# Kernel tuning notes

Measured on AMD Instinct MI355X. Metric: run time of the kernel, lower is better.

Reference implementation:

```python
import jax, jax.numpy as jnp
import numpy as np

B, N, D = 8, 128, 256
EPS = 1e-5


def _layernorm(x, g, b):
    m = jnp.mean(x, axis=-1, keepdims=True)
    v = jnp.mean(jnp.square(x - m), axis=-1, keepdims=True)
    return (x - m) * jax.lax.rsqrt(v + EPS) * g + b


def setup_inputs() -> dict:
    key = jax.random.key(0)
    ks = jax.random.split(key, 24)
    s = 0.05  # param init scale
    return {
        "text": jax.random.normal(ks[0], (B, N, D), jnp.float32),
        "adj1": jax.random.uniform(ks[1], (B, N, N), jnp.float32),
        "adj2": jax.random.uniform(ks[2], (B, N, N), jnp.float32),
        "edge1": jax.random.normal(ks[3], (B, N, N, D), jnp.float32) * 0.1,
        "edge2": jax.random.normal(ks[4], (B, N, N, D), jnp.float32) * 0.1,
        "textmask": jnp.ones((B, N), jnp.float32),
        "weight": jax.random.normal(ks[5], (D, D), jnp.float32) * s,
        "bias": jax.random.normal(ks[6], (D,), jnp.float32) * s,
        "gamma": jnp.ones((D,), jnp.float32),
        "beta": jnp.zeros((D,), jnp.float32),
        "fuse1_w": jax.random.normal(ks[7], (2 * D, D), jnp.float32) * s,
        "fuse2_w": jax.random.normal(ks[8], (2 * D, D), jnp.float32) * s,
        "fc3_w": jax.random.normal(ks[9], (2 * D, D), jnp.float32) * s,
        "fc1_w0": jax.random.normal(ks[10], (3 * D, D), jnp.float32) * s,
        "fc1_w1": jax.random.normal(ks[11], (D, 1), jnp.float32) * s,
        "fc1_b1": jnp.zeros((1,), jnp.float32),
        "fc2_w0": jax.random.normal(ks[12], (3 * D, D), jnp.float32) * s,
        "fc2_w1": jax.random.normal(ks[13], (D, 1), jnp.float32) * s,
        "fc2_b1": jnp.zeros((1,), jnp.float32),
        "align_lin": jax.random.normal(ks[14], (D, D), jnp.float32) * s,
        "align_bias": jax.random.normal(ks[15], (D,), jnp.float32) * s,
    }


def reference(text, adj1, adj2, edge1, edge2, textmask, weight, bias, gamma,
              beta, fuse1_w, fuse2_w, fc3_w, fc1_w0, fc1_w1, fc1_b1,
              fc2_w0, fc2_w1, fc2_b1, align_lin, align_bias):
    d = text.shape[-1]
    # ---- SelfAlignment ----
    logits = jnp.einsum('bid,bjd->bij', text @ align_lin, text)
    mask_add = (1.0 - textmask)[:, None, :] * -1e20
    probs = jax.nn.softmax(logits + mask_add, axis=-1)
    outss = jnp.einsum('bij,bjd->bid', probs, text) * textmask[..., None] + align_bias

    # ---- GCN body ----
    out = jax.nn.relu(text @ weight)  # [B,N,D]

    # edge contributions are loop-invariant: precompute once
    # torch cat([x,e]) @ W  ==  x @ W[:d] + e @ W[d:]
    e1_fuse = jnp.einsum('bijd,de->bije', edge1, fuse1_w[d:])
    e2_fuse = jnp.einsum('bijd,de->bije', edge2, fuse2_w[d:])
    e1_fc = jnp.einsum('bijd,de->bije', edge1, fc1_w0[2 * d:])
    e2_fc = jnp.einsum('bijd,de->bije', edge2, fc2_w0[2 * d:])

    denom1 = jnp.sum(adj1, axis=2, keepdims=True) + 1.0  # [B,N,1]
    denom2 = jnp.sum(adj2, axis=2, keepdims=True) + 1.0

    for _ in range(3):  # K = 3
        # text1[b,i,j] = out[b,i]; text2[b,i,j] = out[b,j]
        t_i1 = (out @ fc1_w0[:d])[:, :, None, :]        # text1 part, fc1
        t_j1 = (out @ fc1_w0[d:2 * d])[:, None, :, :]   # text2 part, fc1
        t_i2 = (out @ fc2_w0[:d])[:, :, None, :]
        t_j2 = (out @ fc2_w0[d:2 * d])[:, None, :, :]

        teout = jax.nn.relu((out @ fuse1_w[:d])[:, None, :, :] + e1_fuse)  # [B,N,N,D]
        tein = jax.nn.relu((out @ fuse2_w[:d])[:, None, :, :] + e2_fuse)

        s1 = jax.nn.sigmoid(jax.nn.relu(t_i1 + t_j1 + e1_fc) @ fc1_w1 + fc1_b1)[..., 0]  # [B,N,N]
        s2 = jax.nn.sigmoid(jax.nn.relu(t_i2 + t_j2 + e2_fc) @ fc2_w1 + fc2_b1)[..., 0]

        out1 = jnp.einsum('bij,bijd->bid', adj1 * s1, teout) / denom1
        out2 = jnp.einsum('bij,bijd->bid', adj2 * s2, tein) / denom2

        out = jax.nn.relu(out1 @ fc3_w[:d] + out2 @ fc3_w[d:]) + out + bias
        out = _layernorm(out, gamma, beta)  # dropout = identity (eval)
    return out, outss
```

## Files before the change

### kernel.cpp

```cpp
#include <hip/hip_runtime.h>

typedef unsigned short u16;
typedef unsigned int u32;
typedef __attribute__((ext_vector_type(8))) short bf16x8;
typedef __attribute__((ext_vector_type(4))) float f32x4;

__device__ __forceinline__ u16 f2bf(float f) {
  u32 u = __float_as_uint(f);
  return (u16)((u + 0x7fffu + ((u >> 16) & 1u)) >> 16);
}
__device__ __forceinline__ float bf2f(u16 h) {
  return __uint_as_float(((u32)h) << 16);
}

template<int K, bool OUT_BF16>
__global__ __launch_bounds__(256) void gemm_mfma(
    const float* __restrict__ A, const u16* __restrict__ Bt,
    void* __restrict__ Cv, int Ntot) {
  constexpr int LD = 72;
  __shared__ __align__(16) u16 Asm[128 * LD];
  __shared__ __align__(16) u16 Bsm[256 * LD];
  const int tid = threadIdx.x;
  const int lane = tid & 63;
  const int w = tid >> 6;
  const int m = lane & 15;
  const int q = lane >> 4;
  const int wrow = (w & 1) * 64;
  const int wcol = (w >> 1) * 128;
  const long rowbase = (long)blockIdx.x * 128;
  const long colbase = (long)blockIdx.y * 256;
  f32x4 acc[4][8];
#pragma unroll
  for (int r = 0; r < 4; ++r)
#pragma unroll
    for (int c = 0; c < 8; ++c) acc[r][c] = (f32x4){0.f, 0.f, 0.f, 0.f};

  for (int kc = 0; kc < K / 64; ++kc) {
    const int kb = kc * 64;
#pragma unroll
    for (int it = 0; it < 8; ++it) {
      int f = it * 256 + tid;
      int r = f >> 4, c4 = (f & 15) * 4;
      float4 v = *(const float4*)(A + (rowbase + r) * K + kb + c4);
      ushort4 h;
      h.x = f2bf(v.x); h.y = f2bf(v.y); h.z = f2bf(v.z); h.w = f2bf(v.w);
      *(ushort4*)&Asm[r * LD + c4] = h;
    }
#pragma unroll
    for (int it = 0; it < 8; ++it) {
      int f = it * 256 + tid;
      int c = f >> 3, k8 = (f & 7) * 8;
      *(uint4*)&Bsm[c * LD + k8] =
          *(const uint4*)(Bt + (colbase + c) * K + kb + k8);
    }
    __syncthreads();
#pragma unroll
    for (int s = 0; s < 2; ++s) {
      const int ko = s * 32 + q * 8;
      bf16x8 av[4], bv[8];
#pragma unroll
      for (int r = 0; r < 4; ++r)
        av[r] = *(const bf16x8*)&Asm[(wrow + r * 16 + m) * LD + ko];
#pragma unroll
      for (int c = 0; c < 8; ++c)
        bv[c] = *(const bf16x8*)&Bsm[(wcol + c * 16 + m) * LD + ko];
#pragma unroll
      for (int r = 0; r < 4; ++r)
#pragma unroll
        for (int c = 0; c < 8; ++c)
          acc[r][c] = __builtin_amdgcn_mfma_f32_16x16x32_bf16(
              av[r], bv[c], acc[r][c], 0, 0, 0);
    }
    __syncthreads();
  }
#pragma unroll
  for (int r = 0; r < 4; ++r)
#pragma unroll
    for (int c = 0; c < 8; ++c)
#pragma unroll
      for (int g = 0; g < 4; ++g) {
        long gr = rowbase + wrow + r * 16 + q * 4 + g;
        long gc = colbase + wcol + c * 16 + m;
        float v = acc[r][c][g];
        if (OUT_BF16) ((u16*)Cv)[gr * Ntot + gc] = f2bf(v);
        else          ((float*)Cv)[gr * Ntot + gc] = v;
      }
}

__global__ __launch_bounds__(256) void prep_bt(
    const float* __restrict__ weight, const float* __restrict__ align_lin,
    const float* __restrict__ fuse1_w, const float* __restrict__ fuse2_w,
    const float* __restrict__ fc1_w0, const float* __restrict__ fc2_w0,
    const float* __restrict__ fc3_w,
    u16* BtE1, u16* BtE2, u16* BtW0, u16* BtLoop, u16* BtFc3) {
  int g = blockIdx.x * 256 + threadIdx.x;
  float v;
  u16* dst;
  if (g < 131072) {
    int c = g >> 8, k = g & 255;
    v = (c < 256) ? fuse1_w[(256 + k) * 256 + c]
                  : fc1_w0[(512 + k) * 256 + (c - 256)];
    dst = BtE1 + g;
  } else if (g < 262144) {
    int t = g - 131072;
    int c = t >> 8, k = t & 255;
    v = (c < 256) ? fuse2_w[(256 + k) * 256 + c]
                  : fc2_w0[(512 + k) * 256 + (c - 256)];
    dst = BtE2 + t;
  } else if (g < 393216) {
    int t = g - 262144;
    int c = t >> 8, k = t & 255;
    v = (c < 256) ? weight[k * 256 + c] : align_lin[k * 256 + (c - 256)];
    dst = BtW0 + t;
  } else if (g < 786432) {
    int t = g - 393216;
    int c = t >> 8, k = t & 255;
    int seg = c >> 8, cc = c & 255;
    if      (seg == 0) v = fuse1_w[k * 256 + cc];
    else if (seg == 1) v = fuse2_w[k * 256 + cc];
    else if (seg == 2) v = fc1_w0[k * 256 + cc];
    else if (seg == 3) v = fc1_w0[(256 + k) * 256 + cc];
    else if (seg == 4) v = fc2_w0[k * 256 + cc];
    else               v = fc2_w0[(256 + k) * 256 + cc];
    dst = BtLoop + t;
  } else {
    int t = g - 786432;
    int c = t >> 9, k = t & 511;
    v = fc3_w[k * 256 + c];
    dst = BtFc3 + t;
  }
  *dst = f2bf(v);
}

__global__ __launch_bounds__(256) void relu0_kernel(const float* __restrict__ T0,
                                                    float* __restrict__ outb) {
  long r = blockIdx.x;
  int d = threadIdx.x;
  outb[r * 256 + d] = fmaxf(T0[r * 512 + d], 0.f);
}

__global__ __launch_bounds__(128) void align_kernel(
    const float* __restrict__ text, const float* __restrict__ T0,
    const float* __restrict__ textmask, const float* __restrict__ align_bias,
    float* __restrict__ outss) {
  const int bi = blockIdx.x;
  const int b = bi >> 7;
  const int tid = threadIdx.x;
  __shared__ float ta[256];
  __shared__ float pr[128];
  __shared__ float red[128];
  ta[tid]       = T0[(long)bi * 512 + 256 + tid];
  ta[tid + 128] = T0[(long)bi * 512 + 384 + tid];
  __syncthreads();
  const float* trow = text + (long)(b * 128 + tid) * 256;
  float dot = 0.f;
  for (int d = 0; d < 256; d += 4) {
    float4 t4 = *(const float4*)(trow + d);
    dot += t4.x * ta[d] + t4.y * ta[d + 1] + t4.z * ta[d + 2] + t4.w * ta[d + 3];
  }
  float logit = dot + (1.0f - textmask[b * 128 + tid]) * -1e20f;
  pr[tid] = logit;
  red[tid] = logit;
  __syncthreads();
  for (int off = 64; off; off >>= 1) {
    if (tid < off) red[tid] = fmaxf(red[tid], red[tid + off]);
    __syncthreads();
  }
  float mx = red[0];
  __syncthreads();
  float e = __expf(pr[tid] - mx);
  red[tid] = e;
  __syncthreads();
  for (int off = 64; off; off >>= 1) {
    if (tid < off) red[tid] += red[tid + off];
    __syncthreads();
  }
  float inv = 1.0f / red[0];
  __syncthreads();
  pr[tid] = e * inv;
  __syncthreads();
  const float mi = textmask[bi];
  for (int h = 0; h < 2; ++h) {
    int d = tid + h * 128;
    float s = 0.f;
    for (int j = 0; j < 128; ++j)
      s += pr[j] * text[(long)(b * 128 + j) * 256 + d];
    outss[(long)bi * 256 + d] = s * mi + align_bias[d];
  }
}

__global__ __launch_bounds__(256) void fused_gate(
    const u16* __restrict__ E1, const u16* __restrict__ E2,
    const float* __restrict__ P, const float* __restrict__ adj1,
    const float* __restrict__ adj2, const float* __restrict__ fc1w1,
    const float* __restrict__ fc1b1, const float* __restrict__ fc2w1,
    const float* __restrict__ fc2b1, float* __restrict__ OU12) {
  const int tid = threadIdx.x, lane = tid & 63, w = tid >> 6;
  const int bi = blockIdx.x;
  const int b = bi >> 7, i = bi & 127;
  const int l4 = lane * 4;
  const float4 w1v = *(const float4*)(fc1w1 + l4);
  const float4 w2v = *(const float4*)(fc2w1 + l4);
  const float b1 = fc1b1[0], b2 = fc2b1[0];
  const long rowi = (long)bi * 1536;
  const float4 ti1 = *(const float4*)(P + rowi + 512 + l4);
  const float4 ti2 = *(const float4*)(P + rowi + 1024 + l4);
  float4 acc1 = {0.f, 0.f, 0.f, 0.f}, acc2 = {0.f, 0.f, 0.f, 0.f};
  float da1 = 0.f, da2 = 0.f;
  const long ebase = ((long)b * 16384 + (long)i * 128) * 512;
  const int abase = b * 16384 + i * 128;
  for (int j = w; j < 128; j += 4) {
    const long er = ebase + (long)j * 512;
    ushort4 e1f = *(const ushort4*)(E1 + er + l4);
    ushort4 e1c = *(const ushort4*)(E1 + er + 256 + l4);
    ushort4 e2f = *(const ushort4*)(E2 + er + l4);
    ushort4 e2c = *(const ushort4*)(E2 + er + 256 + l4);
    const long rowj = (long)(b * 128 + j) * 1536;
    float4 of1 = *(const float4*)(P + rowj + l4);
    float4 of2 = *(const float4*)(P + rowj + 256 + l4);
    float4 tj1 = *(const float4*)(P + rowj + 768 + l4);
    float4 tj2 = *(const float4*)(P + rowj + 1280 + l4);
    float a1 = adj1[abase + j], a2 = adj2[abase + j];
    float z1, z2;
    {
      float r0 = fmaxf(ti1.x + tj1.x + bf2f(e1c.x), 0.f);
      float r1 = fmaxf(ti1.y + tj1.y + bf2f(e1c.y), 0.f);
      float r2 = fmaxf(ti1.z + tj1.z + bf2f(e1c.z), 0.f);
      float r3 = fmaxf(ti1.w + tj1.w + bf2f(e1c.w), 0.f);
      z1 = r0 * w1v.x + r1 * w1v.y + r2 * w1v.z + r3 * w1v.w;
      float s0 = fmaxf(ti2.x + tj2.x + bf2f(e2c.x), 0.f);
      float s1_ = fmaxf(ti2.y + tj2.y + bf2f(e2c.y), 0.f);
      float s2_ = fmaxf(ti2.z + tj2.z + bf2f(e2c.z), 0.f);
      float s3_ = fmaxf(ti2.w + tj2.w + bf2f(e2c.w), 0.f);
      z2 = s0 * w2v.x + s1_ * w2v.y + s2_ * w2v.z + s3_ * w2v.w;
    }
#pragma unroll
    for (int off = 32; off; off >>= 1) {
      z1 += __shfl_xor(z1, off);
      z2 += __shfl_xor(z2, off);
    }
    float s1 = a1 / (1.f + __expf(-(z1 + b1)));
    float s2 = a2 / (1.f + __expf(-(z2 + b2)));
    acc1.x += s1 * fmaxf(of1.x + bf2f(e1f.x), 0.f);
    acc1.y += s1 * fmaxf(of1.y + bf2f(e1f.y), 0.f);
    acc1.z += s1 * fmaxf(of1.z + bf2f(e1f.z), 0.f);
    acc1.w += s1 * fmaxf(of1.w + bf2f(e1f.w), 0.f);
    acc2.x += s2 * fmaxf(of2.x + bf2f(e2f.x), 0.f);
    acc2.y += s2 * fmaxf(of2.y + bf2f(e2f.y), 0.f);
    acc2.z += s2 * fmaxf(of2.z + bf2f(e2f.z), 0.f);
    acc2.w += s2 * fmaxf(of2.w + bf2f(e2f.w), 0.f);
    da1 += a1;
    da2 += a2;
  }
  __shared__ float red[4][512];
  __shared__ float dred[4][2];
  *(float4*)&red[w][l4] = acc1;
  *(float4*)&red[w][256 + l4] = acc2;
  if (lane == 0) { dred[w][0] = da1; dred[w][1] = da2; }
  __syncthreads();
  float o1 = red[0][tid] + red[1][tid] + red[2][tid] + red[3][tid];
  float o2 = red[0][256 + tid] + red[1][256 + tid] + red[2][256 + tid] + red[3][256 + tid];
  float d1 = dred[0][0] + dred[1][0] + dred[2][0] + dred[3][0] + 1.f;
  float d2 = dred[0][1] + dred[1][1] + dred[2][1] + dred[3][1] + 1.f;
  OU12[(long)bi * 512 + tid] = o1 / d1;
  OU12[(long)bi * 512 + 256 + tid] = o2 / d2;
}

__global__ __launch_bounds__(256) void ln_kernel(
    const float* __restrict__ Y, const float* __restrict__ prev,
    const float* __restrict__ bias, const float* __restrict__ gamma,
    const float* __restrict__ beta, float* __restrict__ dst) {
  const int row = blockIdx.x, tid = threadIdx.x, lane = tid & 63, w = tid >> 6;
  const long idx = (long)row * 256 + tid;
  float v = fmaxf(Y[idx], 0.f) + prev[idx] + bias[tid];
  float s = v;
#pragma unroll
  for (int off = 32; off; off >>= 1) s += __shfl_xor(s, off);
  __shared__ float wsA[4], wsB[4];
  if (lane == 0) wsA[w] = s;
  __syncthreads();
  float mean = (wsA[0] + wsA[1] + wsA[2] + wsA[3]) * (1.0f / 256.0f);
  float c = v - mean;
  float s2 = c * c;
#pragma unroll
  for (int off = 32; off; off >>= 1) s2 += __shfl_xor(s2, off);
  if (lane == 0) wsB[w] = s2;
  __syncthreads();
  float var = (wsB[0] + wsB[1] + wsB[2] + wsB[3]) * (1.0f / 256.0f);
  dst[idx] = c * rsqrtf(var + 1e-5f) * gamma[tid] + beta[tid];
}

extern "C" void kernel_launch(void* const* d_in, const int* in_sizes, int n_in,
                              void* d_out, int out_size, void* d_ws, size_t ws_size,
                              hipStream_t stream) {
  const float* text      = (const float*)d_in[0];
  const float* adj1      = (const float*)d_in[1];
  const float* adj2      = (const float*)d_in[2];
  const float* edge1     = (const float*)d_in[3];
  const float* edge2     = (const float*)d_in[4];
  const float* textmask  = (const float*)d_in[5];
  const float* weight    = (const float*)d_in[6];
  const float* bias      = (const float*)d_in[7];
  const float* gamma     = (const float*)d_in[8];
  const float* beta      = (const float*)d_in[9];
  const float* fuse1_w   = (const float*)d_in[10];
  const float* fuse2_w   = (const float*)d_in[11];
  const float* fc3_w     = (const float*)d_in[12];
  const float* fc1_w0    = (const float*)d_in[13];
  const float* fc1_w1    = (const float*)d_in[14];
  const float* fc1_b1    = (const float*)d_in[15];
  const float* fc2_w0    = (const float*)d_in[16];
  const float* fc2_w1    = (const float*)d_in[17];
  const float* fc2_b1    = (const float*)d_in[18];
  const float* align_lin = (const float*)d_in[19];
  const float* align_bias= (const float*)d_in[20];
  float* outF = (float*)d_out;

  char* w8 = (char*)d_ws;
  u16*  E1    = (u16*)w8;
  u16*  E2    = E1 + (long)67108864;
  float* P    = (float*)(w8 + 268435456);
  float* T0   = P + 1572864;
  float* OU12 = T0 + 524288;
  float* outb = OU12 + 524288;
  float* Yb   = outb + 262144;
  u16* BtE1   = (u16*)(Yb + 262144);
  u16* BtE2   = BtE1 + 131072;
  u16* BtW0   = BtE2 + 131072;
  u16* BtLoop = BtW0 + 131072;
  u16* BtFc3  = BtLoop + 393216;

  prep_bt<<<3584, 256, 0, stream>>>(weight, align_lin, fuse1_w, fuse2_w,
                                    fc1_w0, fc2_w0, fc3_w,
                                    BtE1, BtE2, BtW0, BtLoop, BtFc3);
  gemm_mfma<256, true><<<dim3(1024, 2), 256, 0, stream>>>(edge1, BtE1, E1, 512);
  gemm_mfma<256, true><<<dim3(1024, 2), 256, 0, stream>>>(edge2, BtE2, E2, 512);
  gemm_mfma<256, false><<<dim3(8, 2), 256, 0, stream>>>(text, BtW0, T0, 512);
  relu0_kernel<<<1024, 256, 0, stream>>>(T0, outb);
  align_kernel<<<1024, 128, 0, stream>>>(text, T0, textmask, align_bias,
                                         outF + 262144);
  for (int it = 0; it < 3; ++it) {
    gemm_mfma<256, false><<<dim3(8, 6), 256, 0, stream>>>(outb, BtLoop, P, 1536);
    fused_gate<<<1024, 256, 0, stream>>>(E1, E2, P, adj1, adj2, fc1_w1, fc1_b1,
                                         fc2_w1, fc2_b1, OU12);
    gemm_mfma<512, false><<<dim3(8, 1), 256, 0, stream>>>(OU12, BtFc3, Yb, 256);
    ln_kernel<<<1024, 256, 0, stream>>>(Yb, outb, bias, gamma, beta,
                                        (it == 2) ? outF : outb);
  }
}
```

Baseline: 835.8 us.

## Pre-convert edges to swizzled bf16 and use LDS-direct loads in edge GEMM

Edge tensors are first converted to bf16 in a swizzled tiled layout, then a new edge GEMM loads tiles straight into LDS with global_load_lds and XOR-swizzled reads. The fused gate kernel is restructured so each 16-lane group handles one j row with 16 channels per lane and a shorter shuffle reduction. The small GEMMs switch to 64-row tiles to launch more blocks. The separate conversion pass adds a full extra read and write of each edge tensor, and the workspace now aliases P with the conversion buffer.

```diff
diff --git a/kernel.cpp b/kernel.cpp
--- a/kernel.cpp
+++ b/kernel.cpp
@@ -4,6 +4,7 @@
 typedef unsigned int u32;
 typedef __attribute__((ext_vector_type(8))) short bf16x8;
 typedef __attribute__((ext_vector_type(4))) float f32x4;
+typedef __attribute__((ext_vector_type(16))) float f32x16;
 
 __device__ __forceinline__ u16 f2bf(float f) {
   u32 u = __float_as_uint(f);
@@ -13,32 +14,130 @@
   return __uint_as_float(((u32)h) << 16);
 }
 
-template<int K, bool OUT_BF16>
+__device__ __forceinline__ void glds16(const void* g, void* l) {
+  __builtin_amdgcn_global_load_lds(
+      (const __attribute__((address_space(1))) unsigned int*)g,
+      (__attribute__((address_space(3))) unsigned int*)l, 16, 0, 0);
+}
+
+__device__ __forceinline__ f32x16 unpack16(const u16* p) {
+  uint4 a = *(const uint4*)p, b = *(const uint4*)(p + 8);
+  f32x16 r;
+  r[0]  = __uint_as_float(a.x << 16); r[1]  = __uint_as_float(a.x & 0xffff0000u);
+  r[2]  = __uint_as_float(a.y << 16); r[3]  = __uint_as_float(a.y & 0xffff0000u);
+  r[4]  = __uint_as_float(a.z << 16); r[5]  = __uint_as_float(a.z & 0xffff0000u);
+  r[6]  = __uint_as_float(a.w << 16); r[7]  = __uint_as_float(a.w & 0xffff0000u);
+  r[8]  = __uint_as_float(b.x << 16); r[9]  = __uint_as_float(b.x & 0xffff0000u);
+  r[10] = __uint_as_float(b.y << 16); r[11] = __uint_as_float(b.y & 0xffff0000u);
+  r[12] = __uint_as_float(b.z << 16); r[13] = __uint_as_float(b.z & 0xffff0000u);
+  r[14] = __uint_as_float(b.w << 16); r[15] = __uint_as_float(b.w & 0xffff0000u);
+  return r;
+}
+
+__global__ __launch_bounds__(256) void convert_edge(
+    const float* __restrict__ src, u16* __restrict__ dst) {
+  int g = blockIdx.x * 256 + threadIdx.x;
+  int kg = g & 7, r = (g >> 3) & 127, kc = (g >> 10) & 3, rt = g >> 12;
+  const float* s = src + ((long)(rt * 128 + r) * 256 + kc * 64 + kg * 8);
+  float4 a = *(const float4*)s, b = *(const float4*)(s + 4);
+  ushort4 lo, hi;
+  lo.x = f2bf(a.x); lo.y = f2bf(a.y); lo.z = f2bf(a.z); lo.w = f2bf(a.w);
+  hi.x = f2bf(b.x); hi.y = f2bf(b.y); hi.z = f2bf(b.z); hi.w = f2bf(b.w);
+  u16* d = dst + (long)rt * 65536 + kc * 16384 + r * 64 + (kg ^ (r & 7)) * 8;
+  *(ushort4*)d = lo;
+  *(ushort4*)(d + 4) = hi;
+}
+
+__global__ __launch_bounds__(256) void gemm_edge(
+    const u16* __restrict__ A, const u16* __restrict__ Bt,
+    u16* __restrict__ E) {
+  __shared__ __align__(16) u16 Asm[8192];
+  __shared__ __align__(16) u16 Bsm[8192];
+  const int tid = threadIdx.x, lane = tid & 63, w = tid >> 6;
+  const int m = lane & 15, q = lane >> 4;
+  const int rt = blockIdx.x >> 2, ct = blockIdx.x & 3;
+  const int wrow = (w & 1) * 64, wcol = (w >> 1) * 64;
+  const char* Ab = (const char*)A + (long)rt * 131072;
+  const char* Bb = (const char*)Bt + (long)ct * 65536;
+  f32x4 acc[4][4];
+#pragma unroll
+  for (int r = 0; r < 4; ++r)
+#pragma unroll
+    for (int c = 0; c < 4; ++c) acc[r][c] = (f32x4){0.f, 0.f, 0.f, 0.f};
+
+  for (int kc = 0; kc < 4; ++kc) {
+#pragma unroll
+    for (int t = 0; t < 4; ++t) {
+      glds16(Ab + kc * 32768 + t * 4096 + tid * 16,
+             (char*)Asm + t * 4096 + tid * 16);
+      glds16(Bb + kc * 16384 + t * 4096 + tid * 16,
+             (char*)Bsm + t * 4096 + tid * 16);
+    }
+    __syncthreads();
+#pragma unroll
+    for (int s = 0; s < 2; ++s) {
+      const int ko2 = (s * 32 + q * 8) * 2;
+      bf16x8 av[4], bv[4];
+#pragma unroll
+      for (int r = 0; r < 4; ++r) {
+        int row = wrow + r * 16 + m;
+        av[r] = *(const bf16x8*)((const char*)Asm + row * 128 +
+                                 (ko2 ^ ((row & 7) * 16)));
+      }
+#pragma unroll
+      for (int c = 0; c < 4; ++c) {
+        int col = wcol + c * 16 + m;
+        bv[c] = *(const bf16x8*)((const char*)Bsm + col * 128 +
+                                 (ko2 ^ ((col & 7) * 16)));
+      }
+#pragma unroll
+      for (int r = 0; r < 4; ++r)
+#pragma unroll
+        for (int c = 0; c < 4; ++c)
+          acc[r][c] = __builtin_amdgcn_mfma_f32_16x16x32_bf16(
+              av[r], bv[c], acc[r][c], 0, 0, 0);
+    }
+    __syncthreads();
+  }
+#pragma unroll
+  for (int r = 0; r < 4; ++r)
+#pragma unroll
+    for (int c = 0; c < 4; ++c)
+#pragma unroll
+      for (int g = 0; g < 4; ++g) {
+        long gr = (long)rt * 128 + wrow + r * 16 + q * 4 + g;
+        int gc = ct * 128 + wcol + c * 16 + m;
+        E[gr * 512 + gc] = f2bf(acc[r][c][g]);
+      }
+}
+
+template<int K, int ROWS, bool OUT_BF16>
 __global__ __launch_bounds__(256) void gemm_mfma(
     const float* __restrict__ A, const u16* __restrict__ Bt,
     void* __restrict__ Cv, int Ntot) {
   constexpr int LD = 72;
-  __shared__ __align__(16) u16 Asm[128 * LD];
+  constexpr int CF = (ROWS == 128) ? 8 : 4;
+  __shared__ __align__(16) u16 Asm[ROWS * LD];
   __shared__ __align__(16) u16 Bsm[256 * LD];
   const int tid = threadIdx.x;
   const int lane = tid & 63;
   const int w = tid >> 6;
   const int m = lane & 15;
   const int q = lane >> 4;
-  const int wrow = (w & 1) * 64;
-  const int wcol = (w >> 1) * 128;
-  const long rowbase = (long)blockIdx.x * 128;
+  const int wrow = (ROWS == 128) ? (w & 1) * 64 : 0;
+  const int wcol = (ROWS == 128) ? (w >> 1) * 128 : w * 64;
+  const long rowbase = (long)blockIdx.x * ROWS;
   const long colbase = (long)blockIdx.y * 256;
-  f32x4 acc[4][8];
+  f32x4 acc[4][CF];
 #pragma unroll
   for (int r = 0; r < 4; ++r)
 #pragma unroll
-    for (int c = 0; c < 8; ++c) acc[r][c] = (f32x4){0.f, 0.f, 0.f, 0.f};
+    for (int c = 0; c < CF; ++c) acc[r][c] = (f32x4){0.f, 0.f, 0.f, 0.f};
 
   for (int kc = 0; kc < K / 64; ++kc) {
     const int kb = kc * 64;
 #pragma unroll
-    for (int it = 0; it < 8; ++it) {
+    for (int it = 0; it < ROWS / 16; ++it) {
       int f = it * 256 + tid;
       int r = f >> 4, c4 = (f & 15) * 4;
       float4 v = *(const float4*)(A + (rowbase + r) * K + kb + c4);
@@ -57,17 +156,17 @@
 #pragma unroll
     for (int s = 0; s < 2; ++s) {
       const int ko = s * 32 + q * 8;
-      bf16x8 av[4], bv[8];
+      bf16x8 av[4], bv[CF];
 #pragma unroll
       for (int r = 0; r < 4; ++r)
         av[r] = *(const bf16x8*)&Asm[(wrow + r * 16 + m) * LD + ko];
 #pragma unroll
-      for (int c = 0; c < 8; ++c)
+      for (int c = 0; c < CF; ++c)
         bv[c] = *(const bf16x8*)&Bsm[(wcol + c * 16 + m) * LD + ko];
 #pragma unroll
       for (int r = 0; r < 4; ++r)
 #pragma unroll
-        for (int c = 0; c < 8; ++c)
+        for (int c = 0; c < CF; ++c)
           acc[r][c] = __builtin_amdgcn_mfma_f32_16x16x32_bf16(
               av[r], bv[c], acc[r][c], 0, 0, 0);
     }
@@ -76,7 +175,7 @@
 #pragma unroll
   for (int r = 0; r < 4; ++r)
 #pragma unroll
-    for (int c = 0; c < 8; ++c)
+    for (int c = 0; c < CF; ++c)
 #pragma unroll
       for (int g = 0; g < 4; ++g) {
         long gr = rowbase + wrow + r * 16 + q * 4 + g;
@@ -94,42 +193,41 @@
     const float* __restrict__ fc3_w,
     u16* BtE1, u16* BtE2, u16* BtW0, u16* BtLoop, u16* BtFc3) {
   int g = blockIdx.x * 256 + threadIdx.x;
-  float v;
-  u16* dst;
-  if (g < 131072) {
-    int c = g >> 8, k = g & 255;
-    v = (c < 256) ? fuse1_w[(256 + k) * 256 + c]
-                  : fc1_w0[(512 + k) * 256 + (c - 256)];
-    dst = BtE1 + g;
-  } else if (g < 262144) {
-    int t = g - 131072;
-    int c = t >> 8, k = t & 255;
-    v = (c < 256) ? fuse2_w[(256 + k) * 256 + c]
-                  : fc2_w0[(512 + k) * 256 + (c - 256)];
-    dst = BtE2 + t;
+  if (g < 262144) {
+    int t = g & 131071;
+    int col = t >> 8, k = t & 255;
+    float v;
+    if (g < 131072)
+      v = (col < 256) ? fuse1_w[(256 + k) * 256 + col]
+                      : fc1_w0[(512 + k) * 256 + (col - 256)];
+    else
+      v = (col < 256) ? fuse2_w[(256 + k) * 256 + col]
+                      : fc2_w0[(512 + k) * 256 + (col - 256)];
+    int ct = col >> 7, cc = col & 127, kc = k >> 6, kk = k & 63;
+    u16* dst = (g < 131072) ? BtE1 : BtE2;
+    dst[ct * 32768 + kc * 8192 + cc * 64 + (kk ^ ((cc & 7) * 8))] = f2bf(v);
   } else if (g < 393216) {
     int t = g - 262144;
     int c = t >> 8, k = t & 255;
-    v = (c < 256) ? weight[k * 256 + c] : align_lin[k * 256 + (c - 256)];
-    dst = BtW0 + t;
+    float v = (c < 256) ? weight[k * 256 + c] : align_lin[k * 256 + (c - 256)];
+    BtW0[t] = f2bf(v);
   } else if (g < 786432) {
     int t = g - 393216;
     int c = t >> 8, k = t & 255;
     int seg = c >> 8, cc = c & 255;
+    float v;
     if      (seg == 0) v = fuse1_w[k * 256 + cc];
     else if (seg == 1) v = fuse2_w[k * 256 + cc];
     else if (seg == 2) v = fc1_w0[k * 256 + cc];
     else if (seg == 3) v = fc1_w0[(256 + k) * 256 + cc];
     else if (seg == 4) v = fc2_w0[k * 256 + cc];
     else               v = fc2_w0[(256 + k) * 256 + cc];
-    dst = BtLoop + t;
+    BtLoop[t] = f2bf(v);
   } else {
     int t = g - 786432;
     int c = t >> 9, k = t & 511;
-    v = fc3_w[k * 256 + c];
-    dst = BtFc3 + t;
-  }
-  *dst = f2bf(v);
+    BtFc3[t] = f2bf(fc3_w[k * 256 + c]);
+  }
 }
 
 __global__ __launch_bounds__(256) void relu0_kernel(const float* __restrict__ T0,
@@ -196,72 +294,78 @@
     const float* __restrict__ fc1b1, const float* __restrict__ fc2w1,
     const float* __restrict__ fc2b1, float* __restrict__ OU12) {
   const int tid = threadIdx.x, lane = tid & 63, w = tid >> 6;
-  const int bi = blockIdx.x;
-  const int b = bi >> 7, i = bi & 127;
-  const int l4 = lane * 4;
-  const float4 w1v = *(const float4*)(fc1w1 + l4);
-  const float4 w2v = *(const float4*)(fc2w1 + l4);
+  const int g16 = lane >> 4, l16 = lane & 15;
+  const int bi = blockIdx.x, b = bi >> 7;
+  const int db = l16 * 16;
+  const long rowi = (long)bi * 1536;
+  const f32x16 w1v = *(const f32x16*)(fc1w1 + db);
+  const f32x16 w2v = *(const f32x16*)(fc2w1 + db);
+  const f32x16 ti1 = *(const f32x16*)(P + rowi + 512 + db);
+  const f32x16 ti2 = *(const f32x16*)(P + rowi + 1024 + db);
   const float b1 = fc1b1[0], b2 = fc2b1[0];
-  const long rowi = (long)bi * 1536;
-  const float4 ti1 = *(const float4*)(P + rowi + 512 + l4);
-  const float4 ti2 = *(const float4*)(P + rowi + 1024 + l4);
-  float4 acc1 = {0.f, 0.f, 0.f, 0.f}, acc2 = {0.f, 0.f, 0.f, 0.f};
+  const long ebase = (long)bi * 65536;
+  const int abase = bi * 128;
+  f32x16 acc1, acc2;
+#pragma unroll
+  for (int dd = 0; dd < 16; ++dd) { acc1[dd] = 0.f; acc2[dd] = 0.f; }
   float da1 = 0.f, da2 = 0.f;
-  const long ebase = ((long)b * 16384 + (long)i * 128) * 512;
-  const int abase = b * 16384 + i * 128;
-  for (int j = w; j < 128; j += 4) {
+
+  for (int t = 0; t < 8; ++t) {
+    const int j = w * 32 + t * 4 + g16;
     const long er = ebase + (long)j * 512;
-    ushort4 e1f = *(const ushort4*)(E1 + er + l4);
-    ushort4 e1c = *(const ushort4*)(E1 + er + 256 + l4);
-    ushort4 e2f = *(const ushort4*)(E2 + er + l4);
-    ushort4 e2c = *(const ushort4*)(E2 + er + 256 + l4);
     const long rowj = (long)(b * 128 + j) * 1536;
-    float4 of1 = *(const float4*)(P + rowj + l4);
-    float4 of2 = *(const float4*)(P + rowj + 256 + l4);
-    float4 tj1 = *(const float4*)(P + rowj + 768 + l4);
-    float4 tj2 = *(const float4*)(P + rowj + 1280 + l4);
+    f32x16 e1cf = unpack16(E1 + er + 256 + db);
+    f32x16 e2cf = unpack16(E2 + er + 256 + db);
+    f32x16 tj1 = *(const f32x16*)(P + rowj + 768 + db);
+    f32x16 tj2 = *(const f32x16*)(P + rowj + 1280 + db);
     float a1 = adj1[abase + j], a2 = adj2[abase + j];
-    float z1, z2;
-    {
-      float r0 = fmaxf(ti1.x + tj1.x + bf2f(e1c.x), 0.f);
-      float r1 = fmaxf(ti1.y + tj1.y + bf2f(e1c.y), 0.f);
-      float r2 = fmaxf(ti1.z + tj1.z + bf2f(e1c.z), 0.f);
-      float r3 = fmaxf(ti1.w + tj1.w + bf2f(e1c.w), 0.f);
-      z1 = r0 * w1v.x + r1 * w1v.y + r2 * w1v.z + r3 * w1v.w;
-      float s0 = fmaxf(ti2.x + tj2.x + bf2f(e2c.x), 0.f);
-      float s1_ = fmaxf(ti2.y + tj2.y + bf2f(e2c.y), 0.f);
-      float s2_ = fmaxf(ti2.z + tj2.z + bf2f(e2c.z), 0.f);
-      float s3_ = fmaxf(ti2.w + tj2.w + bf2f(e2c.w), 0.f);
-      z2 = s0 * w2v.x + s1_ * w2v.y + s2_ * w2v.z + s3_ * w2v.w;
-    }
-#pragma unroll
-    for (int off = 32; off; off >>= 1) {
+    float z1 = 0.f, z2 = 0.f;
+#pragma unroll
+    for (int dd = 0; dd < 16; ++dd) {
+      z1 += fmaxf(ti1[dd] + tj1[dd] + e1cf[dd], 0.f) * w1v[dd];
+      z2 += fmaxf(ti2[dd] + tj2[dd] + e2cf[dd], 0.f) * w2v[dd];
+    }
+#pragma unroll
+    for (int off = 1; off < 16; off <<= 1) {
       z1 += __shfl_xor(z1, off);
       z2 += __shfl_xor(z2, off);
     }
     float s1 = a1 / (1.f + __expf(-(z1 + b1)));
     float s2 = a2 / (1.f + __expf(-(z2 + b2)));
-    acc1.x += s1 * fmaxf(of1.x + bf2f(e1f.x), 0.f);
-    acc1.y += s1 * fmaxf(of1.y + bf2f(e1f.y), 0.f);
-    acc1.z += s1 * fmaxf(of1.z + bf2f(e1f.z), 0.f);
-    acc1.w += s1 * fmaxf(of1.w + bf2f(e1f.w), 0.f);
-    acc2.x += s2 * fmaxf(of2.x + bf2f(e2f.x), 0.f);
-    acc2.y += s2 * fmaxf(of2.y + bf2f(e2f.y), 0.f);
-    acc2.z += s2 * fmaxf(of2.z + bf2f(e2f.z), 0.f);
-    acc2.w += s2 * fmaxf(of2.w + bf2f(e2f.w), 0.f);
+    f32x16 e1ff = unpack16(E1 + er + db);
+    f32x16 e2ff = unpack16(E2 + er + db);
+    f32x16 of1 = *(const f32x16*)(P + rowj + db);
+    f32x16 of2 = *(const f32x16*)(P + rowj + 256 + db);
+#pragma unroll
+    for (int dd = 0; dd < 16; ++dd) {
+      acc1[dd] += s1 * fmaxf(of1[dd] + e1ff[dd], 0.f);
+      acc2[dd] += s2 * fmaxf(of2[dd] + e2ff[dd], 0.f);
+    }
     da1 += a1;
     da2 += a2;
   }
-  __shared__ float red[4][512];
-  __shared__ float dred[4][2];
-  *(float4*)&red[w][l4] = acc1;
-  *(float4*)&red[w][256 + l4] = acc2;
-  if (lane == 0) { dred[w][0] = da1; dred[w][1] = da2; }
-  __syncthreads();
-  float o1 = red[0][tid] + red[1][tid] + red[2][tid] + red[3][tid];
-  float o2 = red[0][256 + tid] + red[1][256 + tid] + red[2][256 + tid] + red[3][256 + tid];
-  float d1 = dred[0][0] + dred[1][0] + dred[2][0] + dred[3][0] + 1.f;
-  float d2 = dred[0][1] + dred[1][1] + dred[2][1] + dred[3][1] + 1.f;
+
+  __shared__ float redA[16][260];
+  __shared__ float redB[16][260];
+  __shared__ float dA[16], dB[16];
+  const int p = w * 4 + g16;
+#pragma unroll
+  for (int v = 0; v < 4; ++v) {
+    *(float4*)&redA[p][db + v * 4] =
+        make_float4(acc1[v*4], acc1[v*4+1], acc1[v*4+2], acc1[v*4+3]);
+    *(float4*)&redB[p][db + v * 4] =
+        make_float4(acc2[v*4], acc2[v*4+1], acc2[v*4+2], acc2[v*4+3]);
+  }
+  if (l16 == 0) { dA[p] = da1; dB[p] = da2; }
+  __syncthreads();
+  float o1 = 0.f, o2 = 0.f, d1 = 1.f, d2 = 1.f;
+#pragma unroll
+  for (int pp = 0; pp < 16; ++pp) {
+    o1 += redA[pp][tid];
+    o2 += redB[pp][tid];
+    d1 += dA[pp];
+    d2 += dB[pp];
+  }
   OU12[(long)bi * 512 + tid] = o1 / d1;
   OU12[(long)bi * 512 + 256 + tid] = o2 / d2;
 }
@@ -317,33 +421,36 @@
   float* outF = (float*)d_out;
 
   char* w8 = (char*)d_ws;
-  u16*  E1    = (u16*)w8;
-  u16*  E2    = E1 + (long)67108864;
-  float* P    = (float*)(w8 + 268435456);
+  u16* Ax   = (u16*)w8;
+  u16* E1   = (u16*)(w8 + 67108864);
+  u16* E2   = (u16*)(w8 + 201326592);
+  u16* BtE1 = (u16*)(w8 + 335544320);
+  u16* BtE2 = BtE1 + 131072;
+  u16* BtW0 = BtE2 + 131072;
+  u16* BtLoop = BtW0 + 131072;
+  u16* BtFc3  = BtLoop + 393216;
+  float* P    = (float*)w8;
   float* T0   = P + 1572864;
   float* OU12 = T0 + 524288;
   float* outb = OU12 + 524288;
   float* Yb   = outb + 262144;
-  u16* BtE1   = (u16*)(Yb + 262144);
-  u16* BtE2   = BtE1 + 131072;
-  u16* BtW0   = BtE2 + 131072;
-  u16* BtLoop = BtW0 + 131072;
-  u16* BtFc3  = BtLoop + 393216;
 
   prep_bt<<<3584, 256, 0, stream>>>(weight, align_lin, fuse1_w, fuse2_w,
                                     fc1_w0, fc2_w0, fc3_w,
                                     BtE1, BtE2, BtW0, BtLoop, BtFc3);
-  gemm_mfma<256, true><<<dim3(1024, 2), 256, 0, stream>>>(edge1, BtE1, E1, 512);
-  gemm_mfma<256, true><<<dim3(1024, 2), 256, 0, stream>>>(edge2, BtE2, E2, 512);
-  gemm_mfma<256, false><<<dim3(8, 2), 256, 0, stream>>>(text, BtW0, T0, 512);
+  convert_edge<<<16384, 256, 0, stream>>>(edge1, Ax);
+  gemm_edge<<<4096, 256, 0, stream>>>(Ax, BtE1, E1);
+  convert_edge<<<16384, 256, 0, stream>>>(edge2, Ax);
+  gemm_edge<<<4096, 256, 0, stream>>>(Ax, BtE2, E2);
+  gemm_mfma<256, 64, false><<<dim3(16, 2), 256, 0, stream>>>(text, BtW0, T0, 512);
   relu0_kernel<<<1024, 256, 0, stream>>>(T0, outb);
   align_kernel<<<1024, 128, 0, stream>>>(text, T0, textmask, align_bias,
                                          outF + 262144);
   for (int it = 0; it < 3; ++it) {
-    gemm_mfma<256, false><<<dim3(8, 6), 256, 0, stream>>>(outb, BtLoop, P, 1536);
+    gemm_mfma<256, 64, false><<<dim3(16, 6), 256, 0, stream>>>(outb, BtLoop, P, 1536);
     fused_gate<<<1024, 256, 0, stream>>>(E1, E2, P, adj1, adj2, fc1_w1, fc1_b1,
                                          fc2_w1, fc2_b1, OU12);
-    gemm_mfma<512, false><<<dim3(8, 1), 256, 0, stream>>>(OU12, BtFc3, Yb, 256);
+    gemm_mfma<512, 64, false><<<dim3(16, 1), 256, 0, stream>>>(OU12, BtFc3, Yb, 256);
     ln_kernel<<<1024, 256, 0, stream>>>(Yb, outb, bias, gamma, beta,
                                         (it == 2) ? outF : outb);
   }
```

New measurement: 764.2 us. -8.6%, faster.
